# Kernel tuning notes

Hardware: AMD Instinct MI355X
Metric: run time of the kernel (lower is better)

## Reference

```python
import jax, jax.numpy as jnp
import numpy as np

N_NODES = 50000
N_EDGES = 800000
N_GRAPHS = 256
W_SCALE = 0.05  # keep activations bounded through 5 relu conv layers


def setup_inputs() -> dict:
    key = jax.random.key(0)
    ks = jax.random.split(key, 16)
    rn = lambda k, shape: W_SCALE * jax.random.normal(k, shape, dtype=jnp.float32)
    return {
        "x": jax.random.normal(ks[0], (N_NODES, 336), dtype=jnp.float32),
        "edge_index": jax.random.randint(ks[1], (2, N_EDGES), 0, N_NODES, dtype=jnp.int32),
        "batch": jnp.sort(jax.random.randint(ks[2], (N_NODES,), 0, N_GRAPHS, dtype=jnp.int32)),
        "w1_rel": rn(ks[3], (100, 336)),
        "w1_root": rn(ks[4], (100, 336)),
        "b1": rn(ks[5], (100,)),
        "w_rel": rn(ks[6], (4, 100, 100)),
        "w_root": rn(ks[7], (4, 100, 100)),
        "b": rn(ks[8], (4, 100)),
        "lw1": rn(ks[9], (100, 100)),
        "lb1": rn(ks[10], (100,)),
        "lw2": rn(ks[11], (100, 100)),
        "lb2": rn(ks[12], (100,)),
        "lw3": rn(ks[13], (29, 100)),
        "lb3": rn(ks[14], (29,)),
    }


def _graph_conv(x, edge_index, w_rel, w_root, bias):
    # PyG GraphConv: out_i = W_rel @ (sum_{j->i} x_j) + b + W_root @ x_i
    src, dst = edge_index[0], edge_index[1]
    agg = jax.ops.segment_sum(x[src], dst, num_segments=x.shape[0])  # [N, d_in]
    return agg @ w_rel.T + bias + x @ w_root.T


def reference(x, edge_index, batch, w1_rel, w1_root, b1, w_rel, w_root, b,
              lw1, lb1, lw2, lb2, lw3, lb3):
    h = jax.nn.relu(_graph_conv(x, edge_index, w1_rel, w1_root, b1))  # [N,100]
    for i in range(4):  # conv2..conv5 (structurally distinct params)
        h = jax.nn.relu(_graph_conv(h, edge_index, w_rel[i], w_root[i], b[i]))
    # global_mean_pool over graphs
    sums = jax.ops.segment_sum(h, batch, num_segments=N_GRAPHS)          # [G,100]
    counts = jax.ops.segment_sum(jnp.ones((h.shape[0],), h.dtype), batch,
                                 num_segments=N_GRAPHS)                  # [G]
    pooled = sums / jnp.maximum(counts, 1.0)[:, None]
    h = jax.nn.relu(pooled @ lw1.T + lb1)
    h = jax.nn.relu(h @ lw2.T + lb2)
    return h @ lw3.T + lb3  # [G, 29]
```

## Files before the change

kernel.cpp:

```cpp
#include <hip/hip_runtime.h>

#define N_NODES 50000
#define N_EDGES 800000
#define N_GRAPHS 256
#define F 100

#define SCAN_B 512
#define SCAN_NB 98
#define SCAN_PAD (SCAN_NB * SCAN_B)

#define PART_SZ 6250
#define FILL_CHUNK 2048

#define SROW 72
#define EPS 264
#define AST 264

typedef __attribute__((ext_vector_type(8))) short bf16x8;
typedef __attribute__((ext_vector_type(4))) float f32x4;
typedef unsigned short ushort_t;
typedef unsigned int uint_t;

__device__ inline ushort_t f2bf(float f) {
  uint_t u = __float_as_uint(f);
  uint_t r = (u + 0x7fffu + ((u >> 16) & 1u)) >> 16;
  return (ushort_t)r;
}


__global__ __launch_bounds__(256) void hist_kernel(const int* __restrict__ dst,
                                                   int* __restrict__ cnt, int E) {
  int part = blockIdx.x & 7;
  int lo = part * PART_SZ, hi = lo + PART_SZ;
  int base = (blockIdx.x >> 3) * FILL_CHUNK;
  int end = base + FILL_CHUNK; if (end > E) end = E;
  for (int i = base + threadIdx.x; i < end; i += 256) {
    int d = dst[i];
    if (d >= lo && d < hi) atomicAdd(&cnt[d], 1);
  }
}

__global__ __launch_bounds__(SCAN_B) void scan1_kernel(const int* __restrict__ cnt,
                                                       int* __restrict__ excl,
                                                       int* __restrict__ bsum) {
  __shared__ int sh[SCAN_B];
  int t = threadIdx.x;
  int i = blockIdx.x * SCAN_B + t;
  int v = cnt[i];
  sh[t] = v;
  __syncthreads();
  for (int off = 1; off < SCAN_B; off <<= 1) {
    int u = (t >= off) ? sh[t - off] : 0;
    __syncthreads();
    sh[t] += u;
    __syncthreads();
  }
  excl[i] = sh[t] - v;
  if (t == SCAN_B - 1) bsum[blockIdx.x] = sh[t];
}

__global__ __launch_bounds__(128) void scan2_kernel(int* __restrict__ bsum) {
  __shared__ int sh[128];
  int t = threadIdx.x;
  int v = (t < SCAN_NB) ? bsum[t] : 0;
  sh[t] = v;
  __syncthreads();
  for (int off = 1; off < 128; off <<= 1) {
    int u = (t >= off) ? sh[t - off] : 0;
    __syncthreads();
    sh[t] += u;
    __syncthreads();
  }
  if (t < SCAN_NB) bsum[t] = sh[t] - v;
}

__global__ __launch_bounds__(SCAN_B) void scan3_kernel(const int* __restrict__ excl,
                                                       const int* __restrict__ bsum,
                                                       int* __restrict__ offs,
                                                       int* __restrict__ cursor) {
  int i = blockIdx.x * SCAN_B + threadIdx.x;
  int v = excl[i] + bsum[blockIdx.x];
  if (i <= N_NODES) { offs[i] = v; cursor[i] = v; }
}

__global__ __launch_bounds__(256) void fill_kernel(const int* __restrict__ src,
                                                   const int* __restrict__ dst,
                                                   int* __restrict__ cursor,
                                                   int* __restrict__ csr_src, int E) {
  int part = blockIdx.x & 7;
  int lo = part * PART_SZ, hi = lo + PART_SZ;
  int base = (blockIdx.x >> 3) * FILL_CHUNK;
  int end = base + FILL_CHUNK; if (end > E) end = E;
  for (int i = base + threadIdx.x; i < end; i += 256) {
    int d = dst[i];
    if (d >= lo && d < hi) {
      int p = atomicAdd(&cursor[d], 1);
      csr_src[p] = src[i];
    }
  }
}


__global__ void pack_w1_kernel(const float* __restrict__ w1_rel, const float* __restrict__ w1_root,
                               ushort_t* __restrict__ Wp1) {
  int row = blockIdx.x;
  for (int k = threadIdx.x; k < 384; k += 128) {
    float v = 0.f;
    if (k < 336) {
      if (row < 100) v = w1_rel[row * 336 + k];
      else if (row < 200) v = w1_root[(row - 100) * 336 + k];
    }
    Wp1[(size_t)row * 384 + k] = f2bf(v);
  }
}

__global__ void pack_wf_kernel(const float* __restrict__ w_rel, const float* __restrict__ w_root,
                               ushort_t* __restrict__ Wf) {
  int rowl = blockIdx.x;
  int l = rowl >> 7, row = rowl & 127;
  int k = threadIdx.x;
  float v = 0.f;
  if (row < 100) {
    if (k < 100) v = w_rel[((size_t)l * 100 + row) * 100 + k];
    else if (k >= 128 && k < 228) v = w_root[((size_t)l * 100 + row) * 100 + (k - 128)];
  }
  Wf[(size_t)rowl * 256 + k] = f2bf(v);
}


template <bool AF32>
__global__ __launch_bounds__(256) void conv_mfma(
    const void* __restrict__ Aptr, const ushort_t* __restrict__ Wp,
    const float* __restrict__ bias,
    ushort_t* __restrict__ ZP, int Kp) {
  __shared__ short smem[64 * SROW + 208 * SROW];
  __shared__ float bias_s[104];
  short* alds = smem;
  short* blds = smem + 64 * SROW;

  int tid = threadIdx.x;
  int n0 = blockIdx.x * 64;
  if (tid < 100) bias_s[tid] = bias[tid];

  f32x4 acc[13];
#pragma unroll
  for (int b = 0; b < 13; ++b) acc[b] = (f32x4)0.f;

  int w = tid >> 6, lane = tid & 63, q = lane >> 4, m16 = lane & 15;

  int ar[2], aq[2];
#pragma unroll
  for (int u = 0; u < 2; ++u) { int c = tid + u * 256; ar[u] = c >> 3; aq[u] = c & 7; }

  bf16x8 areg[2], breg[7];

  auto load_chunk = [&](int k0) {
#pragma unroll
    for (int u = 0; u < 2; ++u) {
      int node = n0 + ar[u];
      int k = k0 + aq[u] * 8;
      bf16x8 val = (bf16x8)0;
      if (AF32) {
        if (node < N_NODES && k < 336) {
          const float* p = (const float*)Aptr + (size_t)node * 336 + k;
          float4 f0 = *(const float4*)p;
          float4 f1 = *(const float4*)(p + 4);
          val[0] = (short)f2bf(f0.x); val[1] = (short)f2bf(f0.y);
          val[2] = (short)f2bf(f0.z); val[3] = (short)f2bf(f0.w);
          val[4] = (short)f2bf(f1.x); val[5] = (short)f2bf(f1.y);
          val[6] = (short)f2bf(f1.z); val[7] = (short)f2bf(f1.w);
        }
      } else {
        if (node < N_NODES)
          val = *(const bf16x8*)((const short*)Aptr + (size_t)node * 128 + k);
      }
      areg[u] = val;
    }
#pragma unroll
    for (int u = 0; u < 7; ++u) {
      int c = tid + u * 256;
      if (c < 1664) {
        int r = c >> 3, qq = c & 7;
        breg[u] = *(const bf16x8*)((const short*)Wp + (size_t)r * Kp + k0 + qq * 8);
      }
    }
  };

  load_chunk(0);

  for (int k0 = 0; k0 < Kp; k0 += 64) {
#pragma unroll
    for (int u = 0; u < 2; ++u)
      *(bf16x8*)&alds[ar[u] * SROW + aq[u] * 8] = areg[u];
#pragma unroll
    for (int u = 0; u < 7; ++u) {
      int c = tid + u * 256;
      if (c < 1664) {
        int r = c >> 3, qq = c & 7;
        *(bf16x8*)&blds[r * SROW + qq * 8] = breg[u];
      }
    }
    __syncthreads();
    if (k0 + 64 < Kp) load_chunk(k0 + 64);
#pragma unroll
    for (int s = 0; s < 2; ++s) {
      bf16x8 a = *(const bf16x8*)&alds[(w * 16 + m16) * SROW + s * 32 + q * 8];
#pragma unroll
      for (int b = 0; b < 13; ++b) {
        bf16x8 bf = *(const bf16x8*)&blds[(b * 16 + m16) * SROW + s * 32 + q * 8];
        acc[b] = __builtin_amdgcn_mfma_f32_16x16x32_bf16(a, bf, acc[b], 0, 0, 0);
      }
    }
    __syncthreads();
  }

  short* ep = smem;
#pragma unroll
  for (int b = 0; b < 13; ++b) {
    int n = b * 16 + m16;
    if (n < 200) {
      int c = (n < 100) ? n : (n + 28);
      float add = (n < 100) ? 0.f : bias_s[(n - 100) & 127];
#pragma unroll
      for (int r = 0; r < 4; ++r) {
        int row = w * 16 + q * 4 + r;
        ep[row * EPS + c] = (short)f2bf(acc[b][r] + add);
      }
    }
  }
  __syncthreads();
#pragma unroll
  for (int j = 0; j < 8; ++j) {
    int i = tid + j * 256;
    int row = i >> 5, c16 = i & 31;
    int node = n0 + row;
    if (node < N_NODES) {
      *(uint4*)(ZP + (size_t)node * 256 + c16 * 8) =
          *(const uint4*)&ep[row * EPS + c16 * 8];
    }
  }
}


__global__ __launch_bounds__(256) void gather_bf16(
    const ushort_t* __restrict__ ZP,
    const int* __restrict__ offs, const int* __restrict__ csr,
    ushort_t* __restrict__ H) {
  int node = blockIdx.x * 4 + (threadIdx.x >> 6);
  node = __builtin_amdgcn_readfirstlane(node);
  int lane = threadIdx.x & 63;
  int off = (lane < 50 ? lane : 49) * 2;

  uint_t z = *(const uint_t*)(ZP + (size_t)node * 256 + 128 + off);
  float p0[8], p1[8];
#pragma unroll
  for (int u = 0; u < 8; ++u) { p0[u] = 0.f; p1[u] = 0.f; }
  p0[0] = __uint_as_float(z << 16);
  p1[0] = __uint_as_float(z & 0xffff0000u);

  int s = offs[node], e = offs[node + 1];
  for (int j = s; j < e; j += 64) {
    int take = e - j; if (take > 64) take = 64;
    int vidx = (lane < take) ? csr[j + lane] : 0;
    int u = 0;
    for (; u + 8 <= take; u += 8) {
      uint_t zz[8];
#pragma unroll
      for (int t = 0; t < 8; ++t) {
        int idx = __builtin_amdgcn_readlane(vidx, u + t);
        zz[t] = *(const uint_t*)(ZP + (size_t)idx * 256 + off);
      }
#pragma unroll
      for (int t = 0; t < 8; ++t) {
        p0[t] += __uint_as_float(zz[t] << 16);
        p1[t] += __uint_as_float(zz[t] & 0xffff0000u);
      }
    }
    int cnt = take - u;
    if (cnt > 0) {
      uint_t zz[7];
#pragma unroll
      for (int t = 0; t < 7; ++t) {
        if (t < cnt) {
          int idx = __builtin_amdgcn_readlane(vidx, u + t);
          zz[t] = *(const uint_t*)(ZP + (size_t)idx * 256 + off);
        }
      }
#pragma unroll
      for (int t = 0; t < 7; ++t) {
        if (t < cnt) {
          p0[t] += __uint_as_float(zz[t] << 16);
          p1[t] += __uint_as_float(zz[t] & 0xffff0000u);
        }
      }
    }
  }
  float a0 = ((p0[0] + p0[1]) + (p0[2] + p0[3])) + ((p0[4] + p0[5]) + (p0[6] + p0[7]));
  float a1 = ((p1[0] + p1[1]) + (p1[2] + p1[3])) + ((p1[4] + p1[5]) + (p1[6] + p1[7]));
  a0 = fmaxf(a0, 0.f);
  a1 = fmaxf(a1, 0.f);
  uint_t outp = (uint_t)f2bf(a0) | ((uint_t)f2bf(a1) << 16);
  if (lane >= 50) outp = 0u;
  *(uint_t*)(H + (size_t)node * 128 + lane * 2) = outp;
}


__global__ __launch_bounds__(512) void fused_layer(
    const ushort_t* __restrict__ Hin,
    const ushort_t* __restrict__ Wf,
    const float* __restrict__ bias,
    const int* __restrict__ offs, const int* __restrict__ csr,
    ushort_t* __restrict__ Hout) {
  __shared__ short alds[16 * AST];

  int tid = threadIdx.x;
  int w = tid >> 6, lane = tid & 63, q = lane >> 4, m16 = lane & 15;
  int tile = blockIdx.x;

  for (int sub = 0; sub < 2; ++sub) {
    int row = w * 2 + sub;
    int node = tile * 16 + row;
    node = __builtin_amdgcn_readfirstlane(node);
    uint_t hv = *(const uint_t*)(Hin + (size_t)node * 128 + lane * 2);
    *(uint_t*)&alds[row * AST + 128 + lane * 2] = hv;
    int off = (lane < 50 ? lane : 49) * 2;
    float p0[8], p1[8];
#pragma unroll
    for (int u = 0; u < 8; ++u) { p0[u] = 0.f; p1[u] = 0.f; }
    int s = offs[node], e = offs[node + 1];
    for (int j = s; j < e; j += 64) {
      int take = e - j; if (take > 64) take = 64;
      int vidx = (lane < take) ? csr[j + lane] : 0;
      int u = 0;
      for (; u + 8 <= take; u += 8) {
        uint_t zz[8];
#pragma unroll
        for (int t = 0; t < 8; ++t) {
          int idx = __builtin_amdgcn_readlane(vidx, u + t);
          zz[t] = *(const uint_t*)(Hin + (size_t)idx * 128 + off);
        }
#pragma unroll
        for (int t = 0; t < 8; ++t) {
          p0[t] += __uint_as_float(zz[t] << 16);
          p1[t] += __uint_as_float(zz[t] & 0xffff0000u);
        }
      }
      int cnt = take - u;
      if (cnt > 0) {
        uint_t zz[7];
#pragma unroll
        for (int t = 0; t < 7; ++t) {
          if (t < cnt) {
            int idx = __builtin_amdgcn_readlane(vidx, u + t);
            zz[t] = *(const uint_t*)(Hin + (size_t)idx * 128 + off);
          }
        }
#pragma unroll
        for (int t = 0; t < 7; ++t) {
          if (t < cnt) {
            p0[t] += __uint_as_float(zz[t] << 16);
            p1[t] += __uint_as_float(zz[t] & 0xffff0000u);
          }
        }
      }
    }
    float a0 = ((p0[0] + p0[1]) + (p0[2] + p0[3])) + ((p0[4] + p0[5]) + (p0[6] + p0[7]));
    float a1 = ((p1[0] + p1[1]) + (p1[2] + p1[3])) + ((p1[4] + p1[5]) + (p1[6] + p1[7]));
    uint_t outp = (uint_t)f2bf(a0) | ((uint_t)f2bf(a1) << 16);
    if (lane >= 50) outp = 0u;
    *(uint_t*)&alds[row * AST + lane * 2] = outp;
  }

  bf16x8 wreg[8];
#pragma unroll
  for (int s = 0; s < 8; ++s)
    wreg[s] = *(const bf16x8*)(Wf + (size_t)(w * 16 + m16) * 256 + s * 32 + q * 8);
  int n0 = w * 16 + q * 4;
  float4 bb = make_float4(0.f, 0.f, 0.f, 0.f);
  if (n0 < 100) bb = *(const float4*)(bias + n0);

  __syncthreads();

  f32x4 acc = (f32x4)0.f;
#pragma unroll
  for (int s = 0; s < 8; ++s) {
    bf16x8 af = *(const bf16x8*)&alds[m16 * AST + s * 32 + q * 8];
    acc = __builtin_amdgcn_mfma_f32_16x16x32_bf16(wreg[s], af, acc, 0, 0, 0);
  }

  int node = tile * 16 + m16;
  ushort4 v;
  v.x = f2bf(fmaxf(acc[0] + bb.x, 0.f));
  v.y = f2bf(fmaxf(acc[1] + bb.y, 0.f));
  v.z = f2bf(fmaxf(acc[2] + bb.z, 0.f));
  v.w = f2bf(fmaxf(acc[3] + bb.w, 0.f));
  *(ushort4*)(Hout + (size_t)node * 128 + n0) = v;
}


__global__ __launch_bounds__(1024) void pool_kernel(const ushort_t* __restrict__ H,
                                                    const int* __restrict__ batch,
                                                    float* __restrict__ pooled) {
  int g = blockIdx.x;
  int t = threadIdx.x;
  int lo = 0, hi = N_NODES;
  while (lo < hi) { int mid = (lo + hi) >> 1; if (batch[mid] < g) lo = mid + 1; else hi = mid; }
  int s = lo;
  hi = N_NODES;
  while (lo < hi) { int mid = (lo + hi) >> 1; if (batch[mid] <= g) lo = mid + 1; else hi = mid; }
  int e = lo;

  int row = t >> 6;
  int lane = t & 63;
  int off = (lane < 50 ? lane : 49) * 2;
  float a0 = 0.f, a1 = 0.f;
  for (int n = s + row; n < e; n += 16) {
    uint_t z = *(const uint_t*)(H + (size_t)n * 128 + off);
    a0 += __uint_as_float(z << 16);
    a1 += __uint_as_float(z & 0xffff0000u);
  }
  __shared__ float sh[16][104];
  if (lane < 50) { sh[row][lane * 2] = a0; sh[row][lane * 2 + 1] = a1; }
  __syncthreads();
  if (t < 100) {
    float acc = 0.f;
#pragma unroll
    for (int r = 0; r < 16; ++r) acc += sh[r][t];
    int cnt = e - s;
    float d = (cnt > 0) ? (float)cnt : 1.f;
    pooled[(size_t)g * F + t] = acc / d;
  }
}


__global__ void mlp_kernel(const float* __restrict__ pooled,
                           const float* __restrict__ lw1, const float* __restrict__ lb1,
                           const float* __restrict__ lw2, const float* __restrict__ lb2,
                           const float* __restrict__ lw3, const float* __restrict__ lb3,
                           float* __restrict__ out) {
  int g = blockIdx.x;
  int t = threadIdx.x;
  __shared__ float r0[F], r1[F], r2[F];
  if (t < F) r0[t] = pooled[(size_t)g * F + t];
  __syncthreads();
  if (t < F) {
    float s = lb1[t];
    for (int k = 0; k < F; ++k) s += r0[k] * lw1[t * F + k];
    r1[t] = fmaxf(s, 0.f);
  }
  __syncthreads();
  if (t < F) {
    float s = lb2[t];
    for (int k = 0; k < F; ++k) s += r1[k] * lw2[t * F + k];
    r2[t] = fmaxf(s, 0.f);
  }
  __syncthreads();
  if (t < 29) {
    float s = lb3[t];
    for (int k = 0; k < F; ++k) s += r2[k] * lw3[t * F + k];
    out[g * 29 + t] = s;
  }
}


extern "C" void kernel_launch(void* const* d_in, const int* in_sizes, int n_in,
                              void* d_out, int out_size, void* d_ws, size_t ws_size,
                              hipStream_t stream) {
  const float* x       = (const float*)d_in[0];
  const int*   ei      = (const int*)d_in[1];
  const int*   batch   = (const int*)d_in[2];
  const float* w1_rel  = (const float*)d_in[3];
  const float* w1_root = (const float*)d_in[4];
  const float* b1      = (const float*)d_in[5];
  const float* w_rel   = (const float*)d_in[6];
  const float* w_root  = (const float*)d_in[7];
  const float* bvec    = (const float*)d_in[8];
  const float* lw1     = (const float*)d_in[9];
  const float* lb1     = (const float*)d_in[10];
  const float* lw2     = (const float*)d_in[11];
  const float* lb2     = (const float*)d_in[12];
  const float* lw3     = (const float*)d_in[13];
  const float* lb3     = (const float*)d_in[14];
  float* out = (float*)d_out;

  char* ws = (char*)d_ws;
  size_t o = 0;
  auto alloc = [&](size_t bytes) { void* p = ws + o; o = (o + bytes + 511) & ~(size_t)511; return p; };
  ushort_t* H1   = (ushort_t*)alloc((size_t)N_NODES * 128 * 2);
  ushort_t* H2   = (ushort_t*)alloc((size_t)N_NODES * 128 * 2);
  ushort_t* ZP   = (ushort_t*)alloc((size_t)N_NODES * 256 * 2);
  ushort_t* Wp1  = (ushort_t*)alloc((size_t)208 * 384 * 2);
  ushort_t* Wf   = (ushort_t*)alloc((size_t)4 * 128 * 256 * 2);
  float*    pooled = (float*)alloc((size_t)N_GRAPHS * F * 4);
  int* cnt    = (int*)alloc((size_t)SCAN_PAD * 4);
  int* excl   = (int*)alloc((size_t)SCAN_PAD * 4);
  int* bsum   = (int*)alloc((size_t)128 * 4);
  int* offs   = (int*)alloc((size_t)(N_NODES + 1) * 4);
  int* cursor = (int*)alloc((size_t)(N_NODES + 1) * 4);
  int* csr    = (int*)alloc((size_t)N_EDGES * 4);

  const int E = N_EDGES;
  const int* srcv = ei;
  const int* dstv = ei + E;

  int nchunk = (E + FILL_CHUNK - 1) / FILL_CHUNK;
  hipMemsetAsync(cnt, 0, (size_t)SCAN_PAD * sizeof(int), stream);
  hist_kernel<<<nchunk * 8, 256, 0, stream>>>(dstv, cnt, E);
  scan1_kernel<<<SCAN_NB, SCAN_B, 0, stream>>>(cnt, excl, bsum);
  scan2_kernel<<<1, 128, 0, stream>>>(bsum);
  scan3_kernel<<<SCAN_NB, SCAN_B, 0, stream>>>(excl, bsum, offs, cursor);
  fill_kernel<<<nchunk * 8, 256, 0, stream>>>(srcv, dstv, cursor, csr, E);

  pack_w1_kernel<<<208, 128, 0, stream>>>(w1_rel, w1_root, Wp1);
  pack_wf_kernel<<<512, 256, 0, stream>>>(w_rel, w_root, Wf);

  int mmgrid = (N_NODES + 63) / 64;
  conv_mfma<true><<<mmgrid, 256, 0, stream>>>(x, Wp1, b1, ZP, 384);
  gather_bf16<<<N_NODES / 4, 256, 0, stream>>>(ZP, offs, csr, H1);

  const ushort_t* hin = H1;
  ushort_t* hout = H2;
  for (int l = 0; l < 4; ++l) {
    fused_layer<<<N_NODES / 16, 512, 0, stream>>>(hin, Wf + (size_t)l * 128 * 256,
                                                  bvec + (size_t)l * F, offs, csr, hout);
    const ushort_t* tmp = hout; hout = (ushort_t*)hin; hin = tmp;
  }
  pool_kernel<<<N_GRAPHS, 1024, 0, stream>>>(hin, batch, pooled);
  mlp_kernel<<<N_GRAPHS, 128, 0, stream>>>(pooled, lw1, lb1, lw2, lb2, lw3, lb3, out);
}
```

Measured before the change: 457.0 us.

## Merge setup kernels, fuse histogram with first conv, persistent grids

```diff
diff --git a/kernel.cpp b/kernel.cpp
--- a/kernel.cpp
+++ b/kernel.cpp
@@ -5,15 +5,12 @@
 #define N_GRAPHS 256
 #define F 100
 
-#define SCAN_B 512
-#define SCAN_NB 98
-#define SCAN_PAD (SCAN_NB * SCAN_B)
+#define SCAN_PAD 50176
 
 #define PART_SZ 6250
 #define FILL_CHUNK 2048
-
-#define SROW 72
-#define EPS 264
+#define HIST_BLOCKS 3128
+
 #define AST 264
 
 typedef __attribute__((ext_vector_type(8))) short bf16x8;
@@ -28,60 +25,130 @@
 }
 
 
-__global__ __launch_bounds__(256) void hist_kernel(const int* __restrict__ dst,
-                                                   int* __restrict__ cnt, int E) {
-  int part = blockIdx.x & 7;
-  int lo = part * PART_SZ, hi = lo + PART_SZ;
-  int base = (blockIdx.x >> 3) * FILL_CHUNK;
-  int end = base + FILL_CHUNK; if (end > E) end = E;
-  for (int i = base + threadIdx.x; i < end; i += 256) {
-    int d = dst[i];
-    if (d >= lo && d < hi) atomicAdd(&cnt[d], 1);
-  }
-}
-
-__global__ __launch_bounds__(SCAN_B) void scan1_kernel(const int* __restrict__ cnt,
-                                                       int* __restrict__ excl,
-                                                       int* __restrict__ bsum) {
-  __shared__ int sh[SCAN_B];
+__global__ __launch_bounds__(256) void pack_all(
+    const float* __restrict__ w1_rel, const float* __restrict__ w1_root,
+    const float* __restrict__ w_rel, const float* __restrict__ w_root,
+    ushort_t* __restrict__ Wp1, ushort_t* __restrict__ Wf, int* __restrict__ cnt) {
+  int b = blockIdx.x;
+  int tid = threadIdx.x;
+  if (b < 208) {
+    int row = b;
+    for (int k = tid; k < 384; k += 256) {
+      float v = 0.f;
+      if (k < 336) {
+        if (row < 100) v = w1_rel[row * 336 + k];
+        else if (row < 200) v = w1_root[(row - 100) * 336 + k];
+      }
+      Wp1[(size_t)row * 384 + k] = f2bf(v);
+    }
+  } else if (b < 720) {
+    int rowl = b - 208;
+    int l = rowl >> 7, row = rowl & 127;
+    int k = tid;
+    float v = 0.f;
+    if (row < 100) {
+      if (k < 100) v = w_rel[((size_t)l * 100 + row) * 100 + k];
+      else if (k >= 128 && k < 228) v = w_root[((size_t)l * 100 + row) * 100 + (k - 128)];
+    }
+    Wf[(size_t)rowl * 256 + k] = f2bf(v);
+  } else {
+    int z = b - 720;
+    *(int4*)(cnt + (size_t)z * 1024 + tid * 4) = make_int4(0, 0, 0, 0);
+  }
+}
+
+
+__global__ __launch_bounds__(256) void hist_conv(
+    const int* __restrict__ dst, int* __restrict__ cnt, int E,
+    const float* __restrict__ x, const ushort_t* __restrict__ Wp1,
+    const float* __restrict__ b1, ushort_t* __restrict__ ZP) {
+  int tid = threadIdx.x;
+  if (blockIdx.x < HIST_BLOCKS) {
+    int part = blockIdx.x & 7;
+    int lo = part * PART_SZ, hi = lo + PART_SZ;
+    int base = (blockIdx.x >> 3) * FILL_CHUNK;
+    int end = base + FILL_CHUNK; if (end > E) end = E;
+    for (int i = base + tid; i < end; i += 256) {
+      int d = dst[i];
+      if (d >= lo && d < hi) atomicAdd(&cnt[d], 1);
+    }
+    return;
+  }
+  int cb = blockIdx.x - HIST_BLOCKS;
+  int w = tid >> 6, lane = tid & 63, q = lane >> 4, m16 = lane & 15;
+  int gw = cb * 4 + w;
+  for (int tile = gw; tile < 3125; tile += 2048) {
+    int node = tile * 16 + m16;
+    const float* xrow = x + (size_t)node * 336;
+    f32x4 acc[13];
+#pragma unroll
+    for (int b = 0; b < 13; ++b) acc[b] = (f32x4)0.f;
+#pragma unroll
+    for (int s = 0; s < 11; ++s) {
+      int k0 = s * 32 + q * 8;
+      bf16x8 af = (bf16x8)0;
+      if (k0 < 336) {
+        float4 f0 = *(const float4*)(xrow + k0);
+        float4 f1 = *(const float4*)(xrow + k0 + 4);
+        af[0] = (short)f2bf(f0.x); af[1] = (short)f2bf(f0.y);
+        af[2] = (short)f2bf(f0.z); af[3] = (short)f2bf(f0.w);
+        af[4] = (short)f2bf(f1.x); af[5] = (short)f2bf(f1.y);
+        af[6] = (short)f2bf(f1.z); af[7] = (short)f2bf(f1.w);
+      }
+#pragma unroll
+      for (int b = 0; b < 13; ++b) {
+        bf16x8 wf = *(const bf16x8*)(Wp1 + (size_t)(b * 16 + m16) * 384 + s * 32 + q * 8);
+        acc[b] = __builtin_amdgcn_mfma_f32_16x16x32_bf16(wf, af, acc[b], 0, 0, 0);
+      }
+    }
+    size_t zbase = (size_t)node * 256;
+#pragma unroll
+    for (int b = 0; b < 13; ++b) {
+      int n0 = b * 16 + q * 4;
+      if (n0 < 100) {
+        ushort4 v;
+        v.x = f2bf(acc[b][0]); v.y = f2bf(acc[b][1]);
+        v.z = f2bf(acc[b][2]); v.w = f2bf(acc[b][3]);
+        *(ushort4*)(ZP + zbase + n0) = v;
+      } else if (n0 < 200) {
+        float4 bb = *(const float4*)(b1 + n0 - 100);
+        ushort4 v;
+        v.x = f2bf(acc[b][0] + bb.x); v.y = f2bf(acc[b][1] + bb.y);
+        v.z = f2bf(acc[b][2] + bb.z); v.w = f2bf(acc[b][3] + bb.w);
+        *(ushort4*)(ZP + zbase + n0 + 28) = v;
+      }
+    }
+  }
+}
+
+
+__global__ __launch_bounds__(1024) void scan_all(const int* __restrict__ cnt,
+                                                 int* __restrict__ offs,
+                                                 int* __restrict__ cursor) {
+  __shared__ int part[1024];
   int t = threadIdx.x;
-  int i = blockIdx.x * SCAN_B + t;
-  int v = cnt[i];
-  sh[t] = v;
+  int base = t * 49;
+  int s = 0;
+#pragma unroll 7
+  for (int i = 0; i < 49; ++i) s += cnt[base + i];
+  part[t] = s;
   __syncthreads();
-  for (int off = 1; off < SCAN_B; off <<= 1) {
-    int u = (t >= off) ? sh[t - off] : 0;
+  for (int off = 1; off < 1024; off <<= 1) {
+    int u = (t >= off) ? part[t - off] : 0;
     __syncthreads();
-    sh[t] += u;
+    part[t] += u;
     __syncthreads();
   }
-  excl[i] = sh[t] - v;
-  if (t == SCAN_B - 1) bsum[blockIdx.x] = sh[t];
-}
-
-__global__ __launch_bounds__(128) void scan2_kernel(int* __restrict__ bsum) {
-  __shared__ int sh[128];
-  int t = threadIdx.x;
-  int v = (t < SCAN_NB) ? bsum[t] : 0;
-  sh[t] = v;
-  __syncthreads();
-  for (int off = 1; off < 128; off <<= 1) {
-    int u = (t >= off) ? sh[t - off] : 0;
-    __syncthreads();
-    sh[t] += u;
-    __syncthreads();
-  }
-  if (t < SCAN_NB) bsum[t] = sh[t] - v;
-}
-
-__global__ __launch_bounds__(SCAN_B) void scan3_kernel(const int* __restrict__ excl,
-                                                       const int* __restrict__ bsum,
-                                                       int* __restrict__ offs,
-                                                       int* __restrict__ cursor) {
-  int i = blockIdx.x * SCAN_B + threadIdx.x;
-  int v = excl[i] + bsum[blockIdx.x];
-  if (i <= N_NODES) { offs[i] = v; cursor[i] = v; }
-}
+  int run = part[t] - s;
+#pragma unroll 7
+  for (int i = 0; i < 49; ++i) {
+    int idx = base + i;
+    int c = cnt[idx];
+    if (idx <= N_NODES) { offs[idx] = run; cursor[idx] = run; }
+    run += c;
+  }
+}
+
 
 __global__ __launch_bounds__(256) void fill_kernel(const int* __restrict__ src,
                                                    const int* __restrict__ dst,
@@ -101,207 +168,68 @@
 }
 
 
-__global__ void pack_w1_kernel(const float* __restrict__ w1_rel, const float* __restrict__ w1_root,
-                               ushort_t* __restrict__ Wp1) {
-  int row = blockIdx.x;
-  for (int k = threadIdx.x; k < 384; k += 128) {
-    float v = 0.f;
-    if (k < 336) {
-      if (row < 100) v = w1_rel[row * 336 + k];
-      else if (row < 200) v = w1_root[(row - 100) * 336 + k];
-    }
-    Wp1[(size_t)row * 384 + k] = f2bf(v);
-  }
-}
-
-__global__ void pack_wf_kernel(const float* __restrict__ w_rel, const float* __restrict__ w_root,
-                               ushort_t* __restrict__ Wf) {
-  int rowl = blockIdx.x;
-  int l = rowl >> 7, row = rowl & 127;
-  int k = threadIdx.x;
-  float v = 0.f;
-  if (row < 100) {
-    if (k < 100) v = w_rel[((size_t)l * 100 + row) * 100 + k];
-    else if (k >= 128 && k < 228) v = w_root[((size_t)l * 100 + row) * 100 + (k - 128)];
-  }
-  Wf[(size_t)rowl * 256 + k] = f2bf(v);
-}
-
-
-template <bool AF32>
-__global__ __launch_bounds__(256) void conv_mfma(
-    const void* __restrict__ Aptr, const ushort_t* __restrict__ Wp,
-    const float* __restrict__ bias,
-    ushort_t* __restrict__ ZP, int Kp) {
-  __shared__ short smem[64 * SROW + 208 * SROW];
-  __shared__ float bias_s[104];
-  short* alds = smem;
-  short* blds = smem + 64 * SROW;
-
-  int tid = threadIdx.x;
-  int n0 = blockIdx.x * 64;
-  if (tid < 100) bias_s[tid] = bias[tid];
-
-  f32x4 acc[13];
-#pragma unroll
-  for (int b = 0; b < 13; ++b) acc[b] = (f32x4)0.f;
-
-  int w = tid >> 6, lane = tid & 63, q = lane >> 4, m16 = lane & 15;
-
-  int ar[2], aq[2];
-#pragma unroll
-  for (int u = 0; u < 2; ++u) { int c = tid + u * 256; ar[u] = c >> 3; aq[u] = c & 7; }
-
-  bf16x8 areg[2], breg[7];
-
-  auto load_chunk = [&](int k0) {
-#pragma unroll
-    for (int u = 0; u < 2; ++u) {
-      int node = n0 + ar[u];
-      int k = k0 + aq[u] * 8;
-      bf16x8 val = (bf16x8)0;
-      if (AF32) {
-        if (node < N_NODES && k < 336) {
-          const float* p = (const float*)Aptr + (size_t)node * 336 + k;
-          float4 f0 = *(const float4*)p;
-          float4 f1 = *(const float4*)(p + 4);
-          val[0] = (short)f2bf(f0.x); val[1] = (short)f2bf(f0.y);
-          val[2] = (short)f2bf(f0.z); val[3] = (short)f2bf(f0.w);
-          val[4] = (short)f2bf(f1.x); val[5] = (short)f2bf(f1.y);
-          val[6] = (short)f2bf(f1.z); val[7] = (short)f2bf(f1.w);
-        }
-      } else {
-        if (node < N_NODES)
-          val = *(const bf16x8*)((const short*)Aptr + (size_t)node * 128 + k);
-      }
-      areg[u] = val;
-    }
-#pragma unroll
-    for (int u = 0; u < 7; ++u) {
-      int c = tid + u * 256;
-      if (c < 1664) {
-        int r = c >> 3, qq = c & 7;
-        breg[u] = *(const bf16x8*)((const short*)Wp + (size_t)r * Kp + k0 + qq * 8);
-      }
-    }
-  };
-
-  load_chunk(0);
-
-  for (int k0 = 0; k0 < Kp; k0 += 64) {
-#pragma unroll
-    for (int u = 0; u < 2; ++u)
-      *(bf16x8*)&alds[ar[u] * SROW + aq[u] * 8] = areg[u];
-#pragma unroll
-    for (int u = 0; u < 7; ++u) {
-      int c = tid + u * 256;
-      if (c < 1664) {
-        int r = c >> 3, qq = c & 7;
-        *(bf16x8*)&blds[r * SROW + qq * 8] = breg[u];
-      }
-    }
-    __syncthreads();
-    if (k0 + 64 < Kp) load_chunk(k0 + 64);
-#pragma unroll
-    for (int s = 0; s < 2; ++s) {
-      bf16x8 a = *(const bf16x8*)&alds[(w * 16 + m16) * SROW + s * 32 + q * 8];
-#pragma unroll
-      for (int b = 0; b < 13; ++b) {
-        bf16x8 bf = *(const bf16x8*)&blds[(b * 16 + m16) * SROW + s * 32 + q * 8];
-        acc[b] = __builtin_amdgcn_mfma_f32_16x16x32_bf16(a, bf, acc[b], 0, 0, 0);
-      }
-    }
-    __syncthreads();
-  }
-
-  short* ep = smem;
-#pragma unroll
-  for (int b = 0; b < 13; ++b) {
-    int n = b * 16 + m16;
-    if (n < 200) {
-      int c = (n < 100) ? n : (n + 28);
-      float add = (n < 100) ? 0.f : bias_s[(n - 100) & 127];
-#pragma unroll
-      for (int r = 0; r < 4; ++r) {
-        int row = w * 16 + q * 4 + r;
-        ep[row * EPS + c] = (short)f2bf(acc[b][r] + add);
-      }
-    }
-  }
-  __syncthreads();
-#pragma unroll
-  for (int j = 0; j < 8; ++j) {
-    int i = tid + j * 256;
-    int row = i >> 5, c16 = i & 31;
-    int node = n0 + row;
-    if (node < N_NODES) {
-      *(uint4*)(ZP + (size_t)node * 256 + c16 * 8) =
-          *(const uint4*)&ep[row * EPS + c16 * 8];
-    }
-  }
-}
-
-
 __global__ __launch_bounds__(256) void gather_bf16(
     const ushort_t* __restrict__ ZP,
     const int* __restrict__ offs, const int* __restrict__ csr,
     ushort_t* __restrict__ H) {
-  int node = blockIdx.x * 4 + (threadIdx.x >> 6);
-  node = __builtin_amdgcn_readfirstlane(node);
   int lane = threadIdx.x & 63;
   int off = (lane < 50 ? lane : 49) * 2;
-
-  uint_t z = *(const uint_t*)(ZP + (size_t)node * 256 + 128 + off);
-  float p0[8], p1[8];
-#pragma unroll
-  for (int u = 0; u < 8; ++u) { p0[u] = 0.f; p1[u] = 0.f; }
-  p0[0] = __uint_as_float(z << 16);
-  p1[0] = __uint_as_float(z & 0xffff0000u);
-
-  int s = offs[node], e = offs[node + 1];
-  for (int j = s; j < e; j += 64) {
-    int take = e - j; if (take > 64) take = 64;
-    int vidx = (lane < take) ? csr[j + lane] : 0;
-    int u = 0;
-    for (; u + 8 <= take; u += 8) {
-      uint_t zz[8];
-#pragma unroll
-      for (int t = 0; t < 8; ++t) {
-        int idx = __builtin_amdgcn_readlane(vidx, u + t);
-        zz[t] = *(const uint_t*)(ZP + (size_t)idx * 256 + off);
-      }
-#pragma unroll
-      for (int t = 0; t < 8; ++t) {
-        p0[t] += __uint_as_float(zz[t] << 16);
-        p1[t] += __uint_as_float(zz[t] & 0xffff0000u);
-      }
-    }
-    int cnt = take - u;
-    if (cnt > 0) {
-      uint_t zz[7];
-#pragma unroll
-      for (int t = 0; t < 7; ++t) {
-        if (t < cnt) {
+  for (int nb = blockIdx.x; nb < N_NODES / 4; nb += gridDim.x) {
+    int node = nb * 4 + (threadIdx.x >> 6);
+    node = __builtin_amdgcn_readfirstlane(node);
+
+    uint_t z = *(const uint_t*)(ZP + (size_t)node * 256 + 128 + off);
+    float p0[8], p1[8];
+#pragma unroll
+    for (int u = 0; u < 8; ++u) { p0[u] = 0.f; p1[u] = 0.f; }
+    p0[0] = __uint_as_float(z << 16);
+    p1[0] = __uint_as_float(z & 0xffff0000u);
+
+    int s = offs[node], e = offs[node + 1];
+    for (int j = s; j < e; j += 64) {
+      int take = e - j; if (take > 64) take = 64;
+      int vidx = (lane < take) ? csr[j + lane] : 0;
+      int u = 0;
+      for (; u + 8 <= take; u += 8) {
+        uint_t zz[8];
+#pragma unroll
+        for (int t = 0; t < 8; ++t) {
           int idx = __builtin_amdgcn_readlane(vidx, u + t);
           zz[t] = *(const uint_t*)(ZP + (size_t)idx * 256 + off);
         }
-      }
-#pragma unroll
-      for (int t = 0; t < 7; ++t) {
-        if (t < cnt) {
+#pragma unroll
+        for (int t = 0; t < 8; ++t) {
           p0[t] += __uint_as_float(zz[t] << 16);
           p1[t] += __uint_as_float(zz[t] & 0xffff0000u);
         }
       }
-    }
-  }
-  float a0 = ((p0[0] + p0[1]) + (p0[2] + p0[3])) + ((p0[4] + p0[5]) + (p0[6] + p0[7]));
-  float a1 = ((p1[0] + p1[1]) + (p1[2] + p1[3])) + ((p1[4] + p1[5]) + (p1[6] + p1[7]));
-  a0 = fmaxf(a0, 0.f);
-  a1 = fmaxf(a1, 0.f);
-  uint_t outp = (uint_t)f2bf(a0) | ((uint_t)f2bf(a1) << 16);
-  if (lane >= 50) outp = 0u;
-  *(uint_t*)(H + (size_t)node * 128 + lane * 2) = outp;
+      int cnt2 = take - u;
+      if (cnt2 > 0) {
+        uint_t zz[7];
+#pragma unroll
+        for (int t = 0; t < 7; ++t) {
+          if (t < cnt2) {
+            int idx = __builtin_amdgcn_readlane(vidx, u + t);
+            zz[t] = *(const uint_t*)(ZP + (size_t)idx * 256 + off);
+          }
+        }
+#pragma unroll
+        for (int t = 0; t < 7; ++t) {
+          if (t < cnt2) {
+            p0[t] += __uint_as_float(zz[t] << 16);
+            p1[t] += __uint_as_float(zz[t] & 0xffff0000u);
+          }
+        }
+      }
+    }
+    float a0 = ((p0[0] + p0[1]) + (p0[2] + p0[3])) + ((p0[4] + p0[5]) + (p0[6] + p0[7]));
+    float a1 = ((p1[0] + p1[1]) + (p1[2] + p1[3])) + ((p1[4] + p1[5]) + (p1[6] + p1[7]));
+    a0 = fmaxf(a0, 0.f);
+    a1 = fmaxf(a1, 0.f);
+    uint_t outp = (uint_t)f2bf(a0) | ((uint_t)f2bf(a1) << 16);
+    if (lane >= 50) outp = 0u;
+    *(uint_t*)(H + (size_t)node * 128 + lane * 2) = outp;
+  }
 }
 
 
@@ -315,61 +243,6 @@
 
   int tid = threadIdx.x;
   int w = tid >> 6, lane = tid & 63, q = lane >> 4, m16 = lane & 15;
-  int tile = blockIdx.x;
-
-  for (int sub = 0; sub < 2; ++sub) {
-    int row = w * 2 + sub;
-    int node = tile * 16 + row;
-    node = __builtin_amdgcn_readfirstlane(node);
-    uint_t hv = *(const uint_t*)(Hin + (size_t)node * 128 + lane * 2);
-    *(uint_t*)&alds[row * AST + 128 + lane * 2] = hv;
-    int off = (lane < 50 ? lane : 49) * 2;
-    float p0[8], p1[8];
-#pragma unroll
-    for (int u = 0; u < 8; ++u) { p0[u] = 0.f; p1[u] = 0.f; }
-    int s = offs[node], e = offs[node + 1];
-    for (int j = s; j < e; j += 64) {
-      int take = e - j; if (take > 64) take = 64;
-      int vidx = (lane < take) ? csr[j + lane] : 0;
-      int u = 0;
-      for (; u + 8 <= take; u += 8) {
-        uint_t zz[8];
-#pragma unroll
-        for (int t = 0; t < 8; ++t) {
-          int idx = __builtin_amdgcn_readlane(vidx, u + t);
-          zz[t] = *(const uint_t*)(Hin + (size_t)idx * 128 + off);
-        }
-#pragma unroll
-        for (int t = 0; t < 8; ++t) {
-          p0[t] += __uint_as_float(zz[t] << 16);
-          p1[t] += __uint_as_float(zz[t] & 0xffff0000u);
-        }
-      }
-      int cnt = take - u;
-      if (cnt > 0) {
-        uint_t zz[7];
-#pragma unroll
-        for (int t = 0; t < 7; ++t) {
-          if (t < cnt) {
-            int idx = __builtin_amdgcn_readlane(vidx, u + t);
-            zz[t] = *(const uint_t*)(Hin + (size_t)idx * 128 + off);
-          }
-        }
-#pragma unroll
-        for (int t = 0; t < 7; ++t) {
-          if (t < cnt) {
-            p0[t] += __uint_as_float(zz[t] << 16);
-            p1[t] += __uint_as_float(zz[t] & 0xffff0000u);
-          }
-        }
-      }
-    }
-    float a0 = ((p0[0] + p0[1]) + (p0[2] + p0[3])) + ((p0[4] + p0[5]) + (p0[6] + p0[7]));
-    float a1 = ((p1[0] + p1[1]) + (p1[2] + p1[3])) + ((p1[4] + p1[5]) + (p1[6] + p1[7]));
-    uint_t outp = (uint_t)f2bf(a0) | ((uint_t)f2bf(a1) << 16);
-    if (lane >= 50) outp = 0u;
-    *(uint_t*)&alds[row * AST + lane * 2] = outp;
-  }
 
   bf16x8 wreg[8];
 #pragma unroll
@@ -379,28 +252,85 @@
   float4 bb = make_float4(0.f, 0.f, 0.f, 0.f);
   if (n0 < 100) bb = *(const float4*)(bias + n0);
 
-  __syncthreads();
-
-  f32x4 acc = (f32x4)0.f;
-#pragma unroll
-  for (int s = 0; s < 8; ++s) {
-    bf16x8 af = *(const bf16x8*)&alds[m16 * AST + s * 32 + q * 8];
-    acc = __builtin_amdgcn_mfma_f32_16x16x32_bf16(wreg[s], af, acc, 0, 0, 0);
-  }
-
-  int node = tile * 16 + m16;
-  ushort4 v;
-  v.x = f2bf(fmaxf(acc[0] + bb.x, 0.f));
-  v.y = f2bf(fmaxf(acc[1] + bb.y, 0.f));
-  v.z = f2bf(fmaxf(acc[2] + bb.z, 0.f));
-  v.w = f2bf(fmaxf(acc[3] + bb.w, 0.f));
-  *(ushort4*)(Hout + (size_t)node * 128 + n0) = v;
-}
-
-
-__global__ __launch_bounds__(1024) void pool_kernel(const ushort_t* __restrict__ H,
-                                                    const int* __restrict__ batch,
-                                                    float* __restrict__ pooled) {
+  for (int tile = blockIdx.x; tile < 3125; tile += gridDim.x) {
+    for (int sub = 0; sub < 2; ++sub) {
+      int row = w * 2 + sub;
+      int node = tile * 16 + row;
+      node = __builtin_amdgcn_readfirstlane(node);
+      uint_t hv = *(const uint_t*)(Hin + (size_t)node * 128 + lane * 2);
+      *(uint_t*)&alds[row * AST + 128 + lane * 2] = hv;
+      int off = (lane < 50 ? lane : 49) * 2;
+      float p0[8], p1[8];
+#pragma unroll
+      for (int u = 0; u < 8; ++u) { p0[u] = 0.f; p1[u] = 0.f; }
+      int s = offs[node], e = offs[node + 1];
+      for (int j = s; j < e; j += 64) {
+        int take = e - j; if (take > 64) take = 64;
+        int vidx = (lane < take) ? csr[j + lane] : 0;
+        int u = 0;
+        for (; u + 8 <= take; u += 8) {
+          uint_t zz[8];
+#pragma unroll
+          for (int t = 0; t < 8; ++t) {
+            int idx = __builtin_amdgcn_readlane(vidx, u + t);
+            zz[t] = *(const uint_t*)(Hin + (size_t)idx * 128 + off);
+          }
+#pragma unroll
+          for (int t = 0; t < 8; ++t) {
+            p0[t] += __uint_as_float(zz[t] << 16);
+            p1[t] += __uint_as_float(zz[t] & 0xffff0000u);
+          }
+        }
+        int cnt2 = take - u;
+        if (cnt2 > 0) {
+          uint_t zz[7];
+#pragma unroll
+          for (int t = 0; t < 7; ++t) {
+            if (t < cnt2) {
+              int idx = __builtin_amdgcn_readlane(vidx, u + t);
+              zz[t] = *(const uint_t*)(Hin + (size_t)idx * 128 + off);
+            }
+          }
+#pragma unroll
+          for (int t = 0; t < 7; ++t) {
+            if (t < cnt2) {
+              p0[t] += __uint_as_float(zz[t] << 16);
+              p1[t] += __uint_as_float(zz[t] & 0xffff0000u);
+            }
+          }
+        }
+      }
+      float a0 = ((p0[0] + p0[1]) + (p0[2] + p0[3])) + ((p0[4] + p0[5]) + (p0[6] + p0[7]));
+      float a1 = ((p1[0] + p1[1]) + (p1[2] + p1[3])) + ((p1[4] + p1[5]) + (p1[6] + p1[7]));
+      uint_t outp = (uint_t)f2bf(a0) | ((uint_t)f2bf(a1) << 16);
+      if (lane >= 50) outp = 0u;
+      *(uint_t*)&alds[row * AST + lane * 2] = outp;
+    }
+    __syncthreads();
+    f32x4 acc = (f32x4)0.f;
+#pragma unroll
+    for (int s = 0; s < 8; ++s) {
+      bf16x8 af = *(const bf16x8*)&alds[m16 * AST + s * 32 + q * 8];
+      acc = __builtin_amdgcn_mfma_f32_16x16x32_bf16(wreg[s], af, acc, 0, 0, 0);
+    }
+    int nodeo = tile * 16 + m16;
+    ushort4 v;
+    v.x = f2bf(fmaxf(acc[0] + bb.x, 0.f));
+    v.y = f2bf(fmaxf(acc[1] + bb.y, 0.f));
+    v.z = f2bf(fmaxf(acc[2] + bb.z, 0.f));
+    v.w = f2bf(fmaxf(acc[3] + bb.w, 0.f));
+    *(ushort4*)(Hout + (size_t)nodeo * 128 + n0) = v;
+    __syncthreads();
+  }
+}
+
+
+__global__ __launch_bounds__(1024) void pool_mlp(
+    const ushort_t* __restrict__ H, const int* __restrict__ batch,
+    const float* __restrict__ lw1, const float* __restrict__ lb1,
+    const float* __restrict__ lw2, const float* __restrict__ lb2,
+    const float* __restrict__ lw3, const float* __restrict__ lb3,
+    float* __restrict__ out) {
   int g = blockIdx.x;
   int t = threadIdx.x;
   int lo = 0, hi = N_NODES;
@@ -420,45 +350,34 @@
     a1 += __uint_as_float(z & 0xffff0000u);
   }
   __shared__ float sh[16][104];
+  __shared__ float r0[F], r1[F], r2[F];
   if (lane < 50) { sh[row][lane * 2] = a0; sh[row][lane * 2 + 1] = a1; }
   __syncthreads();
-  if (t < 100) {
+  if (t < F) {
     float acc = 0.f;
 #pragma unroll
     for (int r = 0; r < 16; ++r) acc += sh[r][t];
     int cnt = e - s;
     float d = (cnt > 0) ? (float)cnt : 1.f;
-    pooled[(size_t)g * F + t] = acc / d;
-  }
-}
-
-
-__global__ void mlp_kernel(const float* __restrict__ pooled,
-                           const float* __restrict__ lw1, const float* __restrict__ lb1,
-                           const float* __restrict__ lw2, const float* __restrict__ lb2,
-                           const float* __restrict__ lw3, const float* __restrict__ lb3,
-                           float* __restrict__ out) {
-  int g = blockIdx.x;
-  int t = threadIdx.x;
-  __shared__ float r0[F], r1[F], r2[F];
-  if (t < F) r0[t] = pooled[(size_t)g * F + t];
+    r0[t] = acc / d;
+  }
   __syncthreads();
   if (t < F) {
-    float s = lb1[t];
-    for (int k = 0; k < F; ++k) s += r0[k] * lw1[t * F + k];
-    r1[t] = fmaxf(s, 0.f);
+    float sv = lb1[t];
+    for (int k = 0; k < F; ++k) sv += r0[k] * lw1[t * F + k];
+    r1[t] = fmaxf(sv, 0.f);
   }
   __syncthreads();
   if (t < F) {
-    float s = lb2[t];
-    for (int k = 0; k < F; ++k) s += r1[k] * lw2[t * F + k];
-    r2[t] = fmaxf(s, 0.f);
+    float sv = lb2[t];
+    for (int k = 0; k < F; ++k) sv += r1[k] * lw2[t * F + k];
+    r2[t] = fmaxf(sv, 0.f);
   }
   __syncthreads();
   if (t < 29) {
-    float s = lb3[t];
-    for (int k = 0; k < F; ++k) s += r2[k] * lw3[t * F + k];
-    out[g * 29 + t] = s;
+    float sv = lb3[t];
+    for (int k = 0; k < F; ++k) sv += r2[k] * lw3[t * F + k];
+    out[g * 29 + t] = sv;
   }
 }
 
@@ -491,10 +410,7 @@
   ushort_t* ZP   = (ushort_t*)alloc((size_t)N_NODES * 256 * 2);
   ushort_t* Wp1  = (ushort_t*)alloc((size_t)208 * 384 * 2);
   ushort_t* Wf   = (ushort_t*)alloc((size_t)4 * 128 * 256 * 2);
-  float*    pooled = (float*)alloc((size_t)N_GRAPHS * F * 4);
   int* cnt    = (int*)alloc((size_t)SCAN_PAD * 4);
-  int* excl   = (int*)alloc((size_t)SCAN_PAD * 4);
-  int* bsum   = (int*)alloc((size_t)128 * 4);
   int* offs   = (int*)alloc((size_t)(N_NODES + 1) * 4);
   int* cursor = (int*)alloc((size_t)(N_NODES + 1) * 4);
   int* csr    = (int*)alloc((size_t)N_EDGES * 4);
@@ -503,28 +419,18 @@
   const int* srcv = ei;
   const int* dstv = ei + E;
 
-  int nchunk = (E + FILL_CHUNK - 1) / FILL_CHUNK;
-  hipMemsetAsync(cnt, 0, (size_t)SCAN_PAD * sizeof(int), stream);
-  hist_kernel<<<nchunk * 8, 256, 0, stream>>>(dstv, cnt, E);
-  scan1_kernel<<<SCAN_NB, SCAN_B, 0, stream>>>(cnt, excl, bsum);
-  scan2_kernel<<<1, 128, 0, stream>>>(bsum);
-  scan3_kernel<<<SCAN_NB, SCAN_B, 0, stream>>>(excl, bsum, offs, cursor);
-  fill_kernel<<<nchunk * 8, 256, 0, stream>>>(srcv, dstv, cursor, csr, E);
-
-  pack_w1_kernel<<<208, 128, 0, stream>>>(w1_rel, w1_root, Wp1);
-  pack_wf_kernel<<<512, 256, 0, stream>>>(w_rel, w_root, Wf);
-
-  int mmgrid = (N_NODES + 63) / 64;
-  conv_mfma<true><<<mmgrid, 256, 0, stream>>>(x, Wp1, b1, ZP, 384);
-  gather_bf16<<<N_NODES / 4, 256, 0, stream>>>(ZP, offs, csr, H1);
+  pack_all<<<769, 256, 0, stream>>>(w1_rel, w1_root, w_rel, w_root, Wp1, Wf, cnt);
+  hist_conv<<<HIST_BLOCKS + 512, 256, 0, stream>>>(dstv, cnt, E, x, Wp1, b1, ZP);
+  scan_all<<<1, 1024, 0, stream>>>(cnt, offs, cursor);
+  fill_kernel<<<HIST_BLOCKS, 256, 0, stream>>>(srcv, dstv, cursor, csr, E);
+  gather_bf16<<<1024, 256, 0, stream>>>(ZP, offs, csr, H1);
 
   const ushort_t* hin = H1;
   ushort_t* hout = H2;
   for (int l = 0; l < 4; ++l) {
-    fused_layer<<<N_NODES / 16, 512, 0, stream>>>(hin, Wf + (size_t)l * 128 * 256,
-                                                  bvec + (size_t)l * F, offs, csr, hout);
+    fused_layer<<<512, 512, 0, stream>>>(hin, Wf + (size_t)l * 128 * 256,
+                                         bvec + (size_t)l * F, offs, csr, hout);
     const ushort_t* tmp = hout; hout = (ushort_t*)hin; hin = tmp;
   }
-  pool_kernel<<<N_GRAPHS, 1024, 0, stream>>>(hin, batch, pooled);
-  mlp_kernel<<<N_GRAPHS, 128, 0, stream>>>(pooled, lw1, lb1, lw2, lb2, lw3, lb3, out);
-}
+  pool_mlp<<<N_GRAPHS, 1024, 0, stream>>>(hin, batch, lw1, lb1, lw2, lb2, lw3, lb3, out);
+}
```

Result: slower. 651.6 us (+42.6%).
